# Optimization experiments

Hardware: AMD Instinct MI355X
Metric: run time of the kernel (lower is better)

## Reference

```python
import jax, jax.numpy as jnp
import numpy as np

B, C, D = 4, 2048, 1024
DCONV, DMAMBA, K, DSTATE = 512, 512, 4, 16
FFN = 2560


def setup_inputs() -> dict:
    key = jax.random.key(0)
    ks = jax.random.split(key, 16)
    n = lambda k, shape, s=1.0: jax.random.normal(k, shape, jnp.float32) * s
    inv = lambda f: 1.0 / float(np.sqrt(f))
    return {
        "x": n(ks[0], (B, C, D)),
        "velocity": n(ks[1], (B, C, D), 0.1),
        "v_hat_chunk": n(ks[2], (B, C, D)),
        "delta_W": n(ks[3], (FFN, D), 0.01),
        "pre_norm_w": jnp.ones((D,), jnp.float32),
        "ffn_norm_w": jnp.ones((D,), jnp.float32),
        "conv_in_w": n(ks[4], (D, 2 * DCONV), inv(D)),
        "conv_kernel_w": n(ks[5], (K, 1, DCONV), inv(K)),
        "ssm_in_w": n(ks[6], (D, 2 * DMAMBA), inv(D)),
        "ssm_dt_w": n(ks[7], (D, DMAMBA), inv(D)),
        "ssm_dt_b": jnp.full((DMAMBA,), -4.0, jnp.float32),
        "ssm_A_log": jnp.tile(jnp.log(jnp.arange(1.0, DSTATE + 1, dtype=jnp.float32)), (DMAMBA, 1)),
        "ssm_B_w": n(ks[8], (D, DSTATE), inv(D)),
        "ssm_C_w": n(ks[9], (D, DSTATE), inv(D)),
        "ssm_D": jnp.ones((DMAMBA,), jnp.float32),
        "out_proj_w": n(ks[10], (D, D), inv(D)),
        "log_beta": jnp.array(0.0, jnp.float32),  # sigmoid -> beta=0.5
        "ffn_gate_up_w": n(ks[11], (D, 2 * FFN), inv(D)),
        "ffn_down_w": n(ks[12], (FFN, D), inv(FFN)),
        "ffn_target_w": n(ks[13], (D, FFN), inv(D)),
        "log_gamma": jnp.array(0.0, jnp.float32),
        "log_eta": jnp.array(-4.0, jnp.float32),
    }


def _rms(x, w, eps=1e-6):
    return x * jax.lax.rsqrt(jnp.mean(x * x, axis=-1, keepdims=True) + eps) * w


def _gated_conv(xn, w_in, kernel):
    # proj -> split gate/value, depthwise causal conv on value, silu-gate
    g, v = jnp.split(xn @ w_in, 2, axis=-1)  # (B,C,DCONV) each
    v = jax.lax.conv_general_dilated(
        v, kernel, window_strides=(1,), padding=[(K - 1, 0)],
        dimension_numbers=("NWC", "WIO", "NWC"), feature_group_count=DCONV)
    return jax.nn.silu(g) * v


def _ssm(xn, w_in, w_dt, dt_b, A_log, w_B, w_C, Dp):
    # Mamba-style selective SISO scan
    u, z = jnp.split(xn @ w_in, 2, axis=-1)          # (B,C,DMAMBA)
    dt = jax.nn.softplus(xn @ w_dt + dt_b)            # (B,C,DMAMBA)
    A = -jnp.exp(A_log)                               # (DMAMBA,DSTATE)
    Bs = xn @ w_B                                     # (B,C,DSTATE)
    Cs = xn @ w_C                                     # (B,C,DSTATE)
    dA = jnp.exp(dt[..., None] * A)                   # (B,C,DMAMBA,DSTATE)
    dBu = (dt * u)[..., None] * Bs[:, :, None, :]     # (B,C,DMAMBA,DSTATE)

    def step(h, inputs):
        dA_t, dBu_t, C_t = inputs
        h = dA_t * h + dBu_t                          # (B,DMAMBA,DSTATE)
        return h, jnp.einsum("bds,bs->bd", h, C_t)

    xs = (jnp.moveaxis(dA, 1, 0), jnp.moveaxis(dBu, 1, 0), jnp.moveaxis(Cs, 1, 0))
    _, ys = jax.lax.scan(step, jnp.zeros((B, DMAMBA, DSTATE), xn.dtype), xs)
    y = jnp.moveaxis(ys, 0, 1) + Dp * u               # (B,C,DMAMBA)
    return y * jax.nn.silu(z)


def reference(x, velocity, v_hat_chunk, delta_W, pre_norm_w, ffn_norm_w,
              conv_in_w, conv_kernel_w, ssm_in_w, ssm_dt_w, ssm_dt_b, ssm_A_log,
              ssm_B_w, ssm_C_w, ssm_D, out_proj_w, log_beta, ffn_gate_up_w,
              ffn_down_w, ffn_target_w, log_gamma, log_eta):
    xn = _rms(x, pre_norm_w)
    conv_out = _gated_conv(xn, conv_in_w, conv_kernel_w)
    ssm_out = _ssm(xn, ssm_in_w, ssm_dt_w, ssm_dt_b, ssm_A_log, ssm_B_w, ssm_C_w, ssm_D)
    mixed = jnp.concatenate([conv_out, ssm_out], axis=-1) @ out_proj_w
    # momentum residual
    velocity = jax.nn.sigmoid(log_beta) * velocity + mixed
    x = x + velocity
    # Living SwiGLU
    ffn_in = _rms(x, ffn_norm_w)
    gate, up = jnp.split(ffn_in @ ffn_gate_up_w, 2, axis=-1)
    z = jax.nn.silu(gate) * up                        # (B,C,FFN)
    out = z @ ffn_down_w + z @ delta_W                # fast-weight augmented down proj
    v_hat_proj = v_hat_chunk @ ffn_target_w           # (B,C,FFN)
    update = jnp.einsum("bcf,bcd->fd", v_hat_proj, ffn_in) / x.shape[0]
    new_delta_W = jax.nn.sigmoid(log_gamma) * delta_W + jax.nn.softplus(log_eta) * update
    x = x + out
    return (x, velocity, new_delta_W)
```

## Files before the change

kernel.cpp:

```cpp
#include <hip/hip_runtime.h>
#include <stdint.h>
#include <stddef.h>

#define B_ 4
#define C_ 2048
#define D_ 1024
#define FFN_ 2560
#define ROWS_ 8192

typedef unsigned short u16;
typedef short bf16x8 __attribute__((ext_vector_type(8)));
typedef float f32x4 __attribute__((ext_vector_type(4)));

__device__ __forceinline__ float bf2f(u16 x){ union { unsigned u; float f; } v; v.u = ((unsigned)x)<<16; return v.f; }
__device__ __forceinline__ u16 f2bf(float f){ union { float f; unsigned u; } v; v.f = f; unsigned r = v.u + 0x7fffu + ((v.u>>16)&1u); return (u16)(r>>16); }
__device__ __forceinline__ float sigm_(float x){ return 1.f/(1.f+__expf(-x)); }
__device__ __forceinline__ float silu_(float x){ return x/(1.f+__expf(-x)); }
__device__ __forceinline__ float softplus_(float x){ return (x>15.f)? x : log1pf(__expf(x)); }

__device__ __forceinline__ void async16(u16* lds_base, const u16* g){
  __builtin_amdgcn_global_load_lds((const __attribute__((address_space(1))) unsigned int*)g,
                                   (__attribute__((address_space(3))) unsigned int*)lds_base,
                                   16, 0, 0);
}

#define EPI_INPROJ 0
#define EPI_MOM    1
#define EPI_SWIGLU 2
#define EPI_TRANS  3
#define EPI_ATOMX  4
#define EPI_ATOMD  5

template<int EPI>
__global__ __launch_bounds__(256)
void gemm128(const u16* __restrict__ A, const u16* __restrict__ Bt,
             int M, int N, int K, int ksplit,
             float* __restrict__ f0, float* __restrict__ f1,
             const float* __restrict__ c0, const float* __restrict__ c1, const float* __restrict__ c2,
             u16* __restrict__ h0, u16* __restrict__ h1)
{
  __shared__ u16 As[128*32];
  __shared__ u16 Bs[128*32];
  const int tid  = threadIdx.x;
  const int wave = tid>>6, lane = tid&63;
  const int bm = blockIdx.y*128, bn = blockIdx.x*128;
  const int srow = wave*32 + (lane>>2);
  const int scol = (lane&3)*8;
  const u16* aG0 = A  + (size_t)(bm + srow)*K + scol;
  const u16* aG1 = aG0 + (size_t)16*K;
  const u16* bG0 = Bt + (size_t)(bn + srow)*K + scol;
  const u16* bG1 = bG0 + (size_t)16*K;
  u16* aL0 = As + (wave*2+0)*512;
  u16* aL1 = As + (wave*2+1)*512;
  u16* bL0 = Bs + (wave*2+0)*512;
  u16* bL1 = Bs + (wave*2+1)*512;
  const int wr = wave>>1, wc = wave&1;
  const int mrow = lane&15, quad = lane>>4;

  f32x4 acc[4][4];
  #pragma unroll
  for (int i=0;i<4;i++)
    #pragma unroll
    for (int j=0;j<4;j++) acc[i][j] = (f32x4){0.f,0.f,0.f,0.f};

  const int kbeg = blockIdx.z * ksplit;
  const int kend = kbeg + ksplit;
  for (int k0=kbeg; k0<kend; k0+=32){
    __syncthreads();
    async16(aL0, aG0 + k0);
    async16(aL1, aG1 + k0);
    async16(bL0, bG0 + k0);
    async16(bL1, bG1 + k0);
    __syncthreads();
    bf16x8 af[4], bfv[4];
    #pragma unroll
    for (int i=0;i<4;i++) af[i]  = *(const bf16x8*)(As + (wr*64+i*16+mrow)*32 + quad*8);
    #pragma unroll
    for (int j=0;j<4;j++) bfv[j] = *(const bf16x8*)(Bs + (wc*64+j*16+mrow)*32 + quad*8);
    #pragma unroll
    for (int i=0;i<4;i++)
      #pragma unroll
      for (int j=0;j<4;j++)
        acc[i][j] = __builtin_amdgcn_mfma_f32_16x16x32_bf16(af[i], bfv[j], acc[i][j], 0,0,0);
  }

  #pragma unroll
  for (int i=0;i<4;i++){
    const int row0 = bm + wr*64 + i*16 + quad*4;
    #pragma unroll
    for (int j=0;j<4;j++){
      const int col = bn + wc*64 + j*16 + mrow;
      f32x4 v = acc[i][j];
      if constexpr (EPI == EPI_INPROJ){
        if (col < 1024){
          #pragma unroll
          for (int t=0;t<4;t++) h0[(size_t)(row0+t)*1024 + col] = f2bf(v[t]);
        } else if (col < 2048){
          #pragma unroll
          for (int t=0;t<4;t++) h1[(size_t)(row0+t)*1024 + (col-1024)] = f2bf(v[t]);
        } else if (col < 2560){
          const float b = c0[col-2048];
          #pragma unroll
          for (int t=0;t<4;t++) f0[(size_t)(row0+t)*512 + (col-2048)] = softplus_(v[t]+b);
        } else {
          const int cl = col - 2560;
          if (cl < 32){
            #pragma unroll
            for (int t=0;t<4;t++) f1[(size_t)(row0+t)*32 + cl] = v[t];
          }
        }
      } else if constexpr (EPI == EPI_MOM){
        const float beta = sigm_(c2[0]);
        #pragma unroll
        for (int t=0;t<4;t++){
          size_t idx = (size_t)(row0+t)*N + col;
          float vel = beta*c0[idx] + v[t];
          f0[idx] = vel;
          f1[idx] = c1[idx] + vel;
        }
      } else if constexpr (EPI == EPI_SWIGLU){
        float pv[4];
        #pragma unroll
        for (int t=0;t<4;t++) pv[t] = __shfl_xor(v[t], 1, 64);
        if (!(mrow & 1)){
          const int o = col >> 1;
          #pragma unroll
          for (int t=0;t<4;t++) h0[(size_t)(row0+t)*2560 + o] = f2bf(silu_(v[t])*pv[t]);
        }
      } else if constexpr (EPI == EPI_TRANS){
        ushort4 p; p.x=f2bf(v[0]); p.y=f2bf(v[1]); p.z=f2bf(v[2]); p.w=f2bf(v[3]);
        *(ushort4*)(h0 + (size_t)col*M + row0) = p;
      } else if constexpr (EPI == EPI_ATOMX){
        #pragma unroll
        for (int t=0;t<4;t++) atomicAdd(&f0[(size_t)(row0+t)*N + col], v[t]);
      } else if constexpr (EPI == EPI_ATOMD){
        const float e = softplus_(c2[0])*0.25f;
        #pragma unroll
        for (int t=0;t<4;t++) atomicAdd(&f0[(size_t)(row0+t)*N + col], e*v[t]);
      }
    }
  }
}

__global__ void transpose_cvt(const float* __restrict__ W, u16* __restrict__ Wt, int K, int N)
{
  __shared__ float tile[32][33];
  const int tx = threadIdx.x, ty = threadIdx.y;
  const int c0 = blockIdx.x*32, r0 = blockIdx.y*32;
  #pragma unroll
  for (int i=0;i<4;i++) tile[ty+8*i][tx] = W[(size_t)(r0+ty+8*i)*N + c0+tx];
  __syncthreads();
  #pragma unroll
  for (int i=0;i<4;i++) Wt[(size_t)(c0+ty+8*i)*K + r0+tx] = f2bf(tile[tx][ty+8*i]);
}

__global__ void transpose_cvt_gu(const float* __restrict__ W, u16* __restrict__ Wt)
{
  __shared__ float tile[32][33];
  const int tx = threadIdx.x, ty = threadIdx.y;
  const int c0 = blockIdx.x*32, r0 = blockIdx.y*32;
  #pragma unroll
  for (int i=0;i<4;i++) tile[ty+8*i][tx] = W[(size_t)(r0+ty+8*i)*5120 + c0+tx];
  __syncthreads();
  #pragma unroll
  for (int i=0;i<4;i++){
    const int c = c0+ty+8*i;
    const int n = (c < 2560) ? (c*2) : ((c-2560)*2+1);
    Wt[(size_t)n*1024 + r0+tx] = f2bf(tile[tx][ty+8*i]);
  }
}

__global__ void bcw_cvt(const float* __restrict__ Bw, const float* __restrict__ Cw, u16* __restrict__ out)
{
  int i = blockIdx.x*256 + threadIdx.x;
  int r = i >> 10, k = i & 1023;
  float v = 0.f;
  if (r < 16) v = Bw[k*16 + r];
  else if (r < 32) v = Cw[k*16 + (r-16)];
  out[(size_t)r*1024 + k] = f2bf(v);
}

__global__ void weff_transpose(const float* __restrict__ Wa, const float* __restrict__ Wb, u16* __restrict__ Wt)
{
  __shared__ float tile[32][33];
  const int tx = threadIdx.x, ty = threadIdx.y;
  const int c0 = blockIdx.x*32, r0 = blockIdx.y*32;
  #pragma unroll
  for (int i=0;i<4;i++){
    size_t idx = (size_t)(r0+ty+8*i)*1024 + c0+tx;
    tile[ty+8*i][tx] = Wa[idx] + Wb[idx];
  }
  __syncthreads();
  #pragma unroll
  for (int i=0;i<4;i++) Wt[(size_t)(c0+ty+8*i)*2560 + r0+tx] = f2bf(tile[tx][ty+8*i]);
}

__global__ void transpose_bf16(const u16* __restrict__ in, u16* __restrict__ out, int R, int Cc)
{
  __shared__ u16 tile[32][33];
  const int tx = threadIdx.x, ty = threadIdx.y;
  const int c0 = blockIdx.x*32, r0 = blockIdx.y*32;
  #pragma unroll
  for (int i=0;i<4;i++) tile[ty+8*i][tx] = in[(size_t)(r0+ty+8*i)*Cc + c0+tx];
  __syncthreads();
  #pragma unroll
  for (int i=0;i<4;i++) out[(size_t)(c0+ty+8*i)*R + r0+tx] = tile[tx][ty+8*i];
}

__global__ void cvt_bf16x4(const float* __restrict__ in, u16* __restrict__ out, int n4)
{
  int i = blockIdx.x*256 + threadIdx.x;
  if (i < n4){
    float4 v = ((const float4*)in)[i];
    ushort4 p; p.x=f2bf(v.x); p.y=f2bf(v.y); p.z=f2bf(v.z); p.w=f2bf(v.w);
    ((ushort4*)out)[i] = p;
  }
}

__global__ void atab_k(const float* __restrict__ A_log, float* __restrict__ A_tab)
{
  int i = blockIdx.x*256 + threadIdx.x;
  if (i < 512*16) A_tab[i] = -__expf(A_log[i]);
}

__global__ void delta_init(const float* __restrict__ dW, const float* __restrict__ lg, float* __restrict__ out)
{
  int i = blockIdx.x*256 + threadIdx.x;
  float g = sigm_(lg[0]);
  float4 v = ((const float4*)dW)[i];
  float4 r; r.x=g*v.x; r.y=g*v.y; r.z=g*v.z; r.w=g*v.w;
  ((float4*)out)[i] = r;
}

__global__ __launch_bounds__(256) void rmsnorm_k(const float* __restrict__ x, const float* __restrict__ w, u16* __restrict__ out)
{
  const int row = blockIdx.x, tid = threadIdx.x;
  float4 v = ((const float4*)(x + (size_t)row*1024))[tid];
  float s = v.x*v.x + v.y*v.y + v.z*v.z + v.w*v.w;
  #pragma unroll
  for (int o=32;o>0;o>>=1) s += __shfl_down(s, o);
  __shared__ float red[4];
  const int wave = tid>>6, lane = tid&63;
  if (lane==0) red[wave] = s;
  __syncthreads();
  float tot = red[0]+red[1]+red[2]+red[3];
  float sc = rsqrtf(tot*(1.f/1024.f) + 1e-6f);
  float4 wv = ((const float4*)w)[tid];
  ushort4 p; p.x=f2bf(v.x*sc*wv.x); p.y=f2bf(v.y*sc*wv.y); p.z=f2bf(v.z*sc*wv.z); p.w=f2bf(v.w*sc*wv.w);
  ((ushort4*)(out + (size_t)row*1024))[tid] = p;
}

__global__ __launch_bounds__(256) void conv_k(const u16* __restrict__ P1, const float* __restrict__ kw, u16* __restrict__ mixed)
{
  const int idx = blockIdx.x*256 + threadIdx.x;
  const int c = idx & 511;
  const int t = (idx>>9) & 2047;
  const int b = idx >> 20;
  const size_t rowb = (size_t)b*2048;
  float g = bf2f(P1[(rowb+t)*1024 + c]);
  float acc = 0.f;
  #pragma unroll
  for (int k=0;k<4;k++){
    int tt = t-3+k;
    if (tt>=0) acc += bf2f(P1[(rowb+tt)*1024 + 512 + c]) * kw[k*512+c];
  }
  mixed[(rowb+t)*1024 + c] = f2bf(silu_(g)*acc);
}

__global__ __launch_bounds__(256) void scan_p1(const float* __restrict__ dt, const u16* __restrict__ P2,
                                               const float* __restrict__ BCs, const float* __restrict__ A_tab,
                                               float* __restrict__ hend, float* __restrict__ aprod)
{
  const int d = blockIdx.x*256 + threadIdx.x;
  const int ch = blockIdx.y, b = blockIdx.z;
  float Ar[16], h[16], ap[16];
  #pragma unroll
  for (int s=0;s<16;s++){ Ar[s] = A_tab[d*16+s]; h[s]=0.f; ap[s]=1.f; }
  const int t0 = ch*128;
  for (int t=0;t<128;t++){
    size_t row = (size_t)b*2048 + t0 + t;
    float dtv = dt[row*512 + d];
    float u = bf2f(P2[row*1024 + d]);
    float du = dtv*u;
    const float* bs = BCs + row*32;
    #pragma unroll
    for (int s=0;s<16;s++){
      float dA = __expf(dtv*Ar[s]);
      h[s] = dA*h[s] + du*bs[s];
      ap[s] *= dA;
    }
  }
  size_t o = ((size_t)((b*512+d)*16 + ch))*16;
  #pragma unroll
  for (int s=0;s<16;s++){ hend[o+s]=h[s]; aprod[o+s]=ap[s]; }
}

__global__ __launch_bounds__(256) void scan_p2(const float* __restrict__ hend, const float* __restrict__ aprod,
                                               float* __restrict__ hin)
{
  const int g = blockIdx.x*256 + threadIdx.x;
  const int s = g & 15, bd = g >> 4;
  float h = 0.f;
  for (int ch=0; ch<16; ch++){
    size_t o = ((size_t)(bd*16+ch))*16 + s;
    hin[o] = h;
    h = aprod[o]*h + hend[o];
  }
}

__global__ __launch_bounds__(256) void scan_p3(const float* __restrict__ dt, const u16* __restrict__ P2,
                                               const float* __restrict__ BCs, const float* __restrict__ A_tab,
                                               const float* __restrict__ hin, const float* __restrict__ Dp,
                                               u16* __restrict__ mixed)
{
  const int d = blockIdx.x*256 + threadIdx.x;
  const int ch = blockIdx.y, b = blockIdx.z;
  float Ar[16], h[16];
  size_t o = ((size_t)((b*512+d)*16 + ch))*16;
  #pragma unroll
  for (int s=0;s<16;s++){ Ar[s] = A_tab[d*16+s]; h[s] = hin[o+s]; }
  const float Dd = Dp[d];
  const int t0 = ch*128;
  for (int t=0;t<128;t++){
    size_t row = (size_t)b*2048 + t0 + t;
    float dtv = dt[row*512 + d];
    float u = bf2f(P2[row*1024 + d]);
    float zv = bf2f(P2[row*1024 + 512 + d]);
    float du = dtv*u;
    const float* bs = BCs + row*32;
    const float* cs = bs + 16;
    float y = 0.f;
    #pragma unroll
    for (int s=0;s<16;s++){
      float dA = __expf(dtv*Ar[s]);
      h[s] = dA*h[s] + du*bs[s];
      y += h[s]*cs[s];
    }
    float outv = (y + Dd*u)*silu_(zv);
    mixed[row*1024 + 512 + d] = f2bf(outv);
  }
}

extern "C" void kernel_launch(void* const* d_in, const int* in_sizes, int n_in,
                              void* d_out, int out_size, void* d_ws, size_t ws_size,
                              hipStream_t stream)
{
  const float* x          = (const float*)d_in[0];
  const float* velocity   = (const float*)d_in[1];
  const float* v_hat      = (const float*)d_in[2];
  const float* delta_W    = (const float*)d_in[3];
  const float* pre_norm_w = (const float*)d_in[4];
  const float* ffn_norm_w = (const float*)d_in[5];
  const float* conv_in_w  = (const float*)d_in[6];
  const float* conv_kw    = (const float*)d_in[7];
  const float* ssm_in_w   = (const float*)d_in[8];
  const float* ssm_dt_w   = (const float*)d_in[9];
  const float* ssm_dt_b   = (const float*)d_in[10];
  const float* ssm_A_log  = (const float*)d_in[11];
  const float* ssm_B_w    = (const float*)d_in[12];
  const float* ssm_C_w    = (const float*)d_in[13];
  const float* ssm_D      = (const float*)d_in[14];
  const float* out_proj_w = (const float*)d_in[15];
  const float* log_beta   = (const float*)d_in[16];
  const float* gate_up_w  = (const float*)d_in[17];
  const float* ffn_down_w = (const float*)d_in[18];
  const float* ffn_tgt_w  = (const float*)d_in[19];
  const float* log_gamma  = (const float*)d_in[20];
  const float* log_eta    = (const float*)d_in[21];

  float* out_x     = (float*)d_out;
  float* out_vel   = out_x + (size_t)ROWS_*D_;
  float* out_delta = out_vel + (size_t)ROWS_*D_;

  char* wsp = (char*)d_ws;
  size_t off = 0;
  auto alloc = [&](size_t bytes)->char*{ char* p = wsp + off; off += (bytes + 255) & ~(size_t)255; return p; };

  u16* Wti        = (u16*)alloc((size_t)2688*1024*2);
  u16* out_proj_t = (u16*)alloc((size_t)1024*1024*2);
  u16* gate_up_t  = (u16*)alloc((size_t)5120*1024*2);
  u16* target_t   = (u16*)alloc((size_t)2560*1024*2);
  u16* weff_t     = (u16*)alloc((size_t)1024*2560*2);
  float* A_tab    = (float*)alloc((size_t)512*16*4);
  u16* xn         = (u16*)alloc((size_t)ROWS_*1024*2);
  u16* P1         = (u16*)alloc((size_t)ROWS_*1024*2);
  u16* P2         = (u16*)alloc((size_t)ROWS_*1024*2);
  float* dtbuf    = (float*)alloc((size_t)ROWS_*512*4);
  float* BCs      = (float*)alloc((size_t)ROWS_*32*4);
  float* hend     = (float*)alloc((size_t)4*512*16*16*4);
  float* aprod    = (float*)alloc((size_t)4*512*16*16*4);
  float* hin      = (float*)alloc((size_t)4*512*16*16*4);
  u16* mixed      = (u16*)alloc((size_t)ROWS_*1024*2);
  u16* ffn_in     = (u16*)alloc((size_t)ROWS_*1024*2);
  u16* zbuf       = (u16*)alloc((size_t)ROWS_*2560*2);
  u16* T1t        = (u16*)alloc((size_t)2560*ROWS_*2);
  u16* ffn_inT    = xn;
  u16* vhat_bf    = P1;

  dim3 tb(32,8);
  transpose_cvt<<<dim3(32,32),  tb, 0, stream>>>(conv_in_w,  Wti,                    1024, 1024);
  transpose_cvt<<<dim3(32,32),  tb, 0, stream>>>(ssm_in_w,   Wti + (size_t)1024*1024,1024, 1024);
  transpose_cvt<<<dim3(16,32),  tb, 0, stream>>>(ssm_dt_w,   Wti + (size_t)2048*1024,1024, 512);
  bcw_cvt<<<512, 256, 0, stream>>>(ssm_B_w, ssm_C_w, Wti + (size_t)2560*1024);
  transpose_cvt<<<dim3(32,32),  tb, 0, stream>>>(out_proj_w, out_proj_t, 1024, 1024);
  transpose_cvt_gu<<<dim3(160,32), tb, 0, stream>>>(gate_up_w, gate_up_t);
  transpose_cvt<<<dim3(80,32),  tb, 0, stream>>>(ffn_tgt_w,  target_t,  1024, 2560);
  weff_transpose<<<dim3(32,80), tb, 0, stream>>>(ffn_down_w, delta_W, weff_t);
  atab_k<<<32, 256, 0, stream>>>(ssm_A_log, A_tab);
  delta_init<<<2560, 256, 0, stream>>>(delta_W, log_gamma, out_delta);

  rmsnorm_k<<<ROWS_, 256, 0, stream>>>(x, pre_norm_w, xn);
  gemm128<EPI_INPROJ><<<dim3(21,64), 256, 0, stream>>>(xn, Wti, ROWS_,2688,1024,1024,
      dtbuf, BCs, ssm_dt_b, nullptr, nullptr, P1, P2);

  conv_k<<<16384, 256, 0, stream>>>(P1, conv_kw, mixed);
  scan_p1<<<dim3(2,16,4), 256, 0, stream>>>(dtbuf, P2, BCs, A_tab, hend, aprod);
  scan_p2<<<128, 256, 0, stream>>>(hend, aprod, hin);
  scan_p3<<<dim3(2,16,4), 256, 0, stream>>>(dtbuf, P2, BCs, A_tab, hin, ssm_D, mixed);

  gemm128<EPI_MOM><<<dim3(8,64), 256, 0, stream>>>(mixed, out_proj_t, ROWS_,1024,1024,1024,
      out_vel, out_x, velocity, x, log_beta, nullptr, nullptr);

  rmsnorm_k<<<ROWS_, 256, 0, stream>>>(out_x, ffn_norm_w, ffn_in);
  transpose_bf16<<<dim3(32,256), tb, 0, stream>>>(ffn_in, ffn_inT, ROWS_, 1024);
  cvt_bf16x4<<<8192, 256, 0, stream>>>(v_hat, vhat_bf, ROWS_*1024/4);

  gemm128<EPI_SWIGLU><<<dim3(40,64), 256, 0, stream>>>(ffn_in, gate_up_t, ROWS_,5120,1024,1024,
      nullptr,nullptr,nullptr,nullptr,nullptr, zbuf, nullptr);
  gemm128<EPI_TRANS><<<dim3(20,64), 256, 0, stream>>>(vhat_bf, target_t, ROWS_,2560,1024,1024,
      nullptr,nullptr,nullptr,nullptr,nullptr, T1t, nullptr);

  gemm128<EPI_ATOMX><<<dim3(8,64,2), 256, 0, stream>>>(zbuf, weff_t, ROWS_,1024,2560,1280,
      out_x,nullptr,nullptr,nullptr,nullptr, nullptr,nullptr);

  gemm128<EPI_ATOMD><<<dim3(8,20,8), 256, 0, stream>>>(T1t, ffn_inT, 2560,1024,ROWS_,1024,
      out_delta,nullptr,nullptr,nullptr, log_eta, nullptr,nullptr);
}
```

Measured before the change: 979.5 us.

## Shorten scan chunks, stage transposed GEMM epilogue through LDS, merge prep kernels

New measurement: 882.3 us. 9.9% less time.

```diff
diff --git a/kernel.cpp b/kernel.cpp
--- a/kernel.cpp
+++ b/kernel.cpp
@@ -39,8 +39,9 @@
              const float* __restrict__ c0, const float* __restrict__ c1, const float* __restrict__ c2,
              u16* __restrict__ h0, u16* __restrict__ h1)
 {
-  __shared__ u16 As[128*32];
-  __shared__ u16 Bs[128*32];
+  __shared__ u16 smem[8192];
+  u16* As = smem;
+  u16* Bs = smem + 4096;
   const int tid  = threadIdx.x;
   const int wave = tid>>6, lane = tid&63;
   const int bm = blockIdx.y*128, bn = blockIdx.x*128;
@@ -84,100 +85,128 @@
         acc[i][j] = __builtin_amdgcn_mfma_f32_16x16x32_bf16(af[i], bfv[j], acc[i][j], 0,0,0);
   }
 
-  #pragma unroll
-  for (int i=0;i<4;i++){
-    const int row0 = bm + wr*64 + i*16 + quad*4;
-    #pragma unroll
-    for (int j=0;j<4;j++){
-      const int col = bn + wc*64 + j*16 + mrow;
-      f32x4 v = acc[i][j];
-      if constexpr (EPI == EPI_INPROJ){
-        if (col < 1024){
+  if constexpr (EPI == EPI_TRANS){
+    __syncthreads();
+    #pragma unroll
+    for (int h=0; h<4; h++){
+      const int hw = h>>1, j0 = (h&1)*2;
+      if (wc == hw){
+        #pragma unroll
+        for (int i=0;i<4;i++){
+          const int rbase = wr*64 + i*16 + quad*4;
           #pragma unroll
-          for (int t=0;t<4;t++) h0[(size_t)(row0+t)*1024 + col] = f2bf(v[t]);
-        } else if (col < 2048){
-          #pragma unroll
-          for (int t=0;t<4;t++) h1[(size_t)(row0+t)*1024 + (col-1024)] = f2bf(v[t]);
-        } else if (col < 2560){
-          const float b = c0[col-2048];
-          #pragma unroll
-          for (int t=0;t<4;t++) f0[(size_t)(row0+t)*512 + (col-2048)] = softplus_(v[t]+b);
-        } else {
-          const int cl = col - 2560;
-          if (cl < 32){
+          for (int jj=0;jj<2;jj++){
+            const int j = j0+jj;
+            const int cl = jj*16 + mrow;
+            f32x4 v = acc[i][j];
             #pragma unroll
-            for (int t=0;t<4;t++) f1[(size_t)(row0+t)*32 + cl] = v[t];
+            for (int t=0;t<4;t++) smem[cl*132 + rbase + t] = f2bf(v[t]);
           }
         }
-      } else if constexpr (EPI == EPI_MOM){
-        const float beta = sigm_(c2[0]);
+      }
+      __syncthreads();
+      {
+        const int cl2 = tid>>3, m0 = (tid&7)*16;
+        const int col = bn + h*32 + cl2;
+        const ushort4* s4 = (const ushort4*)(smem + cl2*132 + m0);
+        ushort4* d4 = (ushort4*)(h0 + (size_t)col*M + bm + m0);
         #pragma unroll
-        for (int t=0;t<4;t++){
-          size_t idx = (size_t)(row0+t)*N + col;
-          float vel = beta*c0[idx] + v[t];
-          f0[idx] = vel;
-          f1[idx] = c1[idx] + vel;
+        for (int q=0;q<4;q++) d4[q] = s4[q];
+      }
+      __syncthreads();
+    }
+  } else {
+    #pragma unroll
+    for (int i=0;i<4;i++){
+      const int row0 = bm + wr*64 + i*16 + quad*4;
+      if constexpr (EPI == EPI_SWIGLU){
+        #pragma unroll
+        for (int jp=0;jp<4;jp+=2){
+          f32x4 g = acc[i][jp];
+          f32x4 u = acc[i][jp+1];
+          const int o = (((bn + wc*64 + jp*16)>>5)<<4) + mrow;
+          #pragma unroll
+          for (int t=0;t<4;t++) h0[(size_t)(row0+t)*2560 + o] = f2bf(silu_(g[t])*u[t]);
         }
-      } else if constexpr (EPI == EPI_SWIGLU){
-        float pv[4];
+      } else {
         #pragma unroll
-        for (int t=0;t<4;t++) pv[t] = __shfl_xor(v[t], 1, 64);
-        if (!(mrow & 1)){
-          const int o = col >> 1;
-          #pragma unroll
-          for (int t=0;t<4;t++) h0[(size_t)(row0+t)*2560 + o] = f2bf(silu_(v[t])*pv[t]);
+        for (int j=0;j<4;j++){
+          const int col = bn + wc*64 + j*16 + mrow;
+          f32x4 v = acc[i][j];
+          if constexpr (EPI == EPI_INPROJ){
+            if (col < 1024){
+              #pragma unroll
+              for (int t=0;t<4;t++) h0[(size_t)(row0+t)*1024 + col] = f2bf(v[t]);
+            } else if (col < 2048){
+              #pragma unroll
+              for (int t=0;t<4;t++) h1[(size_t)(row0+t)*1024 + (col-1024)] = f2bf(v[t]);
+            } else if (col < 2560){
+              const float b = c0[col-2048];
+              #pragma unroll
+              for (int t=0;t<4;t++) f0[(size_t)(row0+t)*512 + (col-2048)] = softplus_(v[t]+b);
+            } else {
+              const int cl = col - 2560;
+              if (cl < 32){
+                #pragma unroll
+                for (int t=0;t<4;t++) f1[(size_t)(row0+t)*32 + cl] = v[t];
+              }
+            }
+          } else if constexpr (EPI == EPI_MOM){
+            const float beta = sigm_(c2[0]);
+            #pragma unroll
+            for (int t=0;t<4;t++){
+              size_t idx = (size_t)(row0+t)*N + col;
+              float vel = beta*c0[idx] + v[t];
+              f0[idx] = vel;
+              f1[idx] = c1[idx] + vel;
+            }
+          } else if constexpr (EPI == EPI_ATOMX){
+            #pragma unroll
+            for (int t=0;t<4;t++) atomicAdd(&f0[(size_t)(row0+t)*N + col], v[t]);
+          } else if constexpr (EPI == EPI_ATOMD){
+            const float e = softplus_(c2[0])*0.25f;
+            #pragma unroll
+            for (int t=0;t<4;t++) atomicAdd(&f0[(size_t)(row0+t)*N + col], e*v[t]);
+          }
         }
-      } else if constexpr (EPI == EPI_TRANS){
-        ushort4 p; p.x=f2bf(v[0]); p.y=f2bf(v[1]); p.z=f2bf(v[2]); p.w=f2bf(v[3]);
-        *(ushort4*)(h0 + (size_t)col*M + row0) = p;
-      } else if constexpr (EPI == EPI_ATOMX){
-        #pragma unroll
-        for (int t=0;t<4;t++) atomicAdd(&f0[(size_t)(row0+t)*N + col], v[t]);
-      } else if constexpr (EPI == EPI_ATOMD){
-        const float e = softplus_(c2[0])*0.25f;
-        #pragma unroll
-        for (int t=0;t<4;t++) atomicAdd(&f0[(size_t)(row0+t)*N + col], e*v[t]);
       }
     }
   }
 }
 
-__global__ void transpose_cvt(const float* __restrict__ W, u16* __restrict__ Wt, int K, int N)
-{
+__global__ void prep_transposes(const float* __restrict__ conv_in_w, const float* __restrict__ ssm_in_w,
+                                const float* __restrict__ ssm_dt_w, const float* __restrict__ out_proj_w,
+                                const float* __restrict__ ffn_tgt_w, const float* __restrict__ gate_up_w,
+                                u16* __restrict__ Wti, u16* __restrict__ out_proj_t,
+                                u16* __restrict__ target_t, u16* __restrict__ gate_up_t)
+{
+  const int z = blockIdx.z;
+  const float* W; u16* Wt; int N; bool gu = false;
+  switch(z){
+    case 0: W=conv_in_w;  Wt=Wti;                       N=1024; break;
+    case 1: W=ssm_in_w;   Wt=Wti + (size_t)1024*1024;   N=1024; break;
+    case 2: W=ssm_dt_w;   Wt=Wti + (size_t)2048*1024;   N=512;  break;
+    case 3: W=out_proj_w; Wt=out_proj_t;                N=1024; break;
+    case 4: W=ffn_tgt_w;  Wt=target_t;                  N=2560; break;
+    default: W=gate_up_w; Wt=gate_up_t;                 N=5120; gu=true; break;
+  }
+  const int c0 = blockIdx.x*32, r0 = blockIdx.y*32;
+  if (c0 >= N) return;
   __shared__ float tile[32][33];
   const int tx = threadIdx.x, ty = threadIdx.y;
-  const int c0 = blockIdx.x*32, r0 = blockIdx.y*32;
   #pragma unroll
   for (int i=0;i<4;i++) tile[ty+8*i][tx] = W[(size_t)(r0+ty+8*i)*N + c0+tx];
   __syncthreads();
   #pragma unroll
-  for (int i=0;i<4;i++) Wt[(size_t)(c0+ty+8*i)*K + r0+tx] = f2bf(tile[tx][ty+8*i]);
-}
-
-__global__ void transpose_cvt_gu(const float* __restrict__ W, u16* __restrict__ Wt)
-{
-  __shared__ float tile[32][33];
-  const int tx = threadIdx.x, ty = threadIdx.y;
-  const int c0 = blockIdx.x*32, r0 = blockIdx.y*32;
-  #pragma unroll
-  for (int i=0;i<4;i++) tile[ty+8*i][tx] = W[(size_t)(r0+ty+8*i)*5120 + c0+tx];
-  __syncthreads();
-  #pragma unroll
   for (int i=0;i<4;i++){
     const int c = c0+ty+8*i;
-    const int n = (c < 2560) ? (c*2) : ((c-2560)*2+1);
+    int n;
+    if (gu){
+      if (c < 2560) n = ((c>>4)<<5) | (c&15);
+      else { int o = c-2560; n = ((o>>4)<<5) | 16 | (o&15); }
+    } else n = c;
     Wt[(size_t)n*1024 + r0+tx] = f2bf(tile[tx][ty+8*i]);
   }
-}
-
-__global__ void bcw_cvt(const float* __restrict__ Bw, const float* __restrict__ Cw, u16* __restrict__ out)
-{
-  int i = blockIdx.x*256 + threadIdx.x;
-  int r = i >> 10, k = i & 1023;
-  float v = 0.f;
-  if (r < 16) v = Bw[k*16 + r];
-  else if (r < 32) v = Cw[k*16 + (r-16)];
-  out[(size_t)r*1024 + k] = f2bf(v);
 }
 
 __global__ void weff_transpose(const float* __restrict__ Wa, const float* __restrict__ Wb, u16* __restrict__ Wt)
@@ -217,19 +246,30 @@
   }
 }
 
-__global__ void atab_k(const float* __restrict__ A_log, float* __restrict__ A_tab)
-{
-  int i = blockIdx.x*256 + threadIdx.x;
-  if (i < 512*16) A_tab[i] = -__expf(A_log[i]);
-}
-
-__global__ void delta_init(const float* __restrict__ dW, const float* __restrict__ lg, float* __restrict__ out)
-{
-  int i = blockIdx.x*256 + threadIdx.x;
-  float g = sigm_(lg[0]);
-  float4 v = ((const float4*)dW)[i];
-  float4 r; r.x=g*v.x; r.y=g*v.y; r.z=g*v.z; r.w=g*v.w;
-  ((float4*)out)[i] = r;
+__global__ void prep_small(const float* __restrict__ dW, const float* __restrict__ lg,
+                           const float* __restrict__ Bw, const float* __restrict__ Cw,
+                           const float* __restrict__ A_log,
+                           float* __restrict__ out_delta, u16* __restrict__ bc_dst,
+                           float* __restrict__ A_tab)
+{
+  const int blk = blockIdx.x, tid = threadIdx.x;
+  if (blk < 2560){
+    int i = blk*256 + tid;
+    float g = sigm_(lg[0]);
+    float4 v = ((const float4*)dW)[i];
+    float4 r; r.x=g*v.x; r.y=g*v.y; r.z=g*v.z; r.w=g*v.w;
+    ((float4*)out_delta)[i] = r;
+  } else if (blk < 3072){
+    int i = (blk-2560)*256 + tid;
+    int r = i >> 10, k = i & 1023;
+    float v = 0.f;
+    if (r < 16) v = Bw[k*16 + r];
+    else if (r < 32) v = Cw[k*16 + (r-16)];
+    bc_dst[(size_t)r*1024 + k] = f2bf(v);
+  } else {
+    int i = (blk-3072)*256 + tid;
+    if (i < 512*16) A_tab[i] = -__expf(A_log[i]);
+  }
 }
 
 __global__ __launch_bounds__(256) void rmsnorm_k(const float* __restrict__ x, const float* __restrict__ w, u16* __restrict__ out)
@@ -267,6 +307,8 @@
   mixed[(rowb+t)*1024 + c] = f2bf(silu_(g)*acc);
 }
 
+#define NCH_ 64
+#define CHL_ 32
 __global__ __launch_bounds__(256) void scan_p1(const float* __restrict__ dt, const u16* __restrict__ P2,
                                                const float* __restrict__ BCs, const float* __restrict__ A_tab,
                                                float* __restrict__ hend, float* __restrict__ aprod)
@@ -276,8 +318,8 @@
   float Ar[16], h[16], ap[16];
   #pragma unroll
   for (int s=0;s<16;s++){ Ar[s] = A_tab[d*16+s]; h[s]=0.f; ap[s]=1.f; }
-  const int t0 = ch*128;
-  for (int t=0;t<128;t++){
+  const int t0 = ch*CHL_;
+  for (int t=0;t<CHL_;t++){
     size_t row = (size_t)b*2048 + t0 + t;
     float dtv = dt[row*512 + d];
     float u = bf2f(P2[row*1024 + d]);
@@ -290,21 +332,21 @@
       ap[s] *= dA;
     }
   }
-  size_t o = ((size_t)((b*512+d)*16 + ch))*16;
+  size_t o = ((size_t)((b*512+d)*NCH_ + ch))*16;
   #pragma unroll
   for (int s=0;s<16;s++){ hend[o+s]=h[s]; aprod[o+s]=ap[s]; }
 }
 
-__global__ __launch_bounds__(256) void scan_p2(const float* __restrict__ hend, const float* __restrict__ aprod,
-                                               float* __restrict__ hin)
+__global__ __launch_bounds__(256) void scan_p2(float* __restrict__ hend, const float* __restrict__ aprod)
 {
   const int g = blockIdx.x*256 + threadIdx.x;
   const int s = g & 15, bd = g >> 4;
   float h = 0.f;
-  for (int ch=0; ch<16; ch++){
-    size_t o = ((size_t)(bd*16+ch))*16 + s;
-    hin[o] = h;
-    h = aprod[o]*h + hend[o];
+  for (int ch=0; ch<NCH_; ch++){
+    size_t o = ((size_t)(bd*NCH_+ch))*16 + s;
+    float he = hend[o], ap = aprod[o];
+    hend[o] = h;
+    h = ap*h + he;
   }
 }
 
@@ -316,12 +358,12 @@
   const int d = blockIdx.x*256 + threadIdx.x;
   const int ch = blockIdx.y, b = blockIdx.z;
   float Ar[16], h[16];
-  size_t o = ((size_t)((b*512+d)*16 + ch))*16;
+  size_t o = ((size_t)((b*512+d)*NCH_ + ch))*16;
   #pragma unroll
   for (int s=0;s<16;s++){ Ar[s] = A_tab[d*16+s]; h[s] = hin[o+s]; }
   const float Dd = Dp[d];
-  const int t0 = ch*128;
-  for (int t=0;t<128;t++){
+  const int t0 = ch*CHL_;
+  for (int t=0;t<CHL_;t++){
     size_t row = (size_t)b*2048 + t0 + t;
     float dtv = dt[row*512 + d];
     float u = bf2f(P2[row*1024 + d]);
@@ -387,9 +429,8 @@
   u16* P2         = (u16*)alloc((size_t)ROWS_*1024*2);
   float* dtbuf    = (float*)alloc((size_t)ROWS_*512*4);
   float* BCs      = (float*)alloc((size_t)ROWS_*32*4);
-  float* hend     = (float*)alloc((size_t)4*512*16*16*4);
-  float* aprod    = (float*)alloc((size_t)4*512*16*16*4);
-  float* hin      = (float*)alloc((size_t)4*512*16*16*4);
+  float* hend     = (float*)alloc((size_t)4*512*NCH_*16*4);
+  float* aprod    = (float*)alloc((size_t)4*512*NCH_*16*4);
   u16* mixed      = (u16*)alloc((size_t)ROWS_*1024*2);
   u16* ffn_in     = (u16*)alloc((size_t)ROWS_*1024*2);
   u16* zbuf       = (u16*)alloc((size_t)ROWS_*2560*2);
@@ -398,25 +439,20 @@
   u16* vhat_bf    = P1;
 
   dim3 tb(32,8);
-  transpose_cvt<<<dim3(32,32),  tb, 0, stream>>>(conv_in_w,  Wti,                    1024, 1024);
-  transpose_cvt<<<dim3(32,32),  tb, 0, stream>>>(ssm_in_w,   Wti + (size_t)1024*1024,1024, 1024);
-  transpose_cvt<<<dim3(16,32),  tb, 0, stream>>>(ssm_dt_w,   Wti + (size_t)2048*1024,1024, 512);
-  bcw_cvt<<<512, 256, 0, stream>>>(ssm_B_w, ssm_C_w, Wti + (size_t)2560*1024);
-  transpose_cvt<<<dim3(32,32),  tb, 0, stream>>>(out_proj_w, out_proj_t, 1024, 1024);
-  transpose_cvt_gu<<<dim3(160,32), tb, 0, stream>>>(gate_up_w, gate_up_t);
-  transpose_cvt<<<dim3(80,32),  tb, 0, stream>>>(ffn_tgt_w,  target_t,  1024, 2560);
+  prep_transposes<<<dim3(160,32,6), tb, 0, stream>>>(conv_in_w, ssm_in_w, ssm_dt_w, out_proj_w,
+      ffn_tgt_w, gate_up_w, Wti, out_proj_t, target_t, gate_up_t);
   weff_transpose<<<dim3(32,80), tb, 0, stream>>>(ffn_down_w, delta_W, weff_t);
-  atab_k<<<32, 256, 0, stream>>>(ssm_A_log, A_tab);
-  delta_init<<<2560, 256, 0, stream>>>(delta_W, log_gamma, out_delta);
+  prep_small<<<3104, 256, 0, stream>>>(delta_W, log_gamma, ssm_B_w, ssm_C_w, ssm_A_log,
+      out_delta, Wti + (size_t)2560*1024, A_tab);
 
   rmsnorm_k<<<ROWS_, 256, 0, stream>>>(x, pre_norm_w, xn);
   gemm128<EPI_INPROJ><<<dim3(21,64), 256, 0, stream>>>(xn, Wti, ROWS_,2688,1024,1024,
       dtbuf, BCs, ssm_dt_b, nullptr, nullptr, P1, P2);
 
   conv_k<<<16384, 256, 0, stream>>>(P1, conv_kw, mixed);
-  scan_p1<<<dim3(2,16,4), 256, 0, stream>>>(dtbuf, P2, BCs, A_tab, hend, aprod);
-  scan_p2<<<128, 256, 0, stream>>>(hend, aprod, hin);
-  scan_p3<<<dim3(2,16,4), 256, 0, stream>>>(dtbuf, P2, BCs, A_tab, hin, ssm_D, mixed);
+  scan_p1<<<dim3(2,NCH_,4), 256, 0, stream>>>(dtbuf, P2, BCs, A_tab, hend, aprod);
+  scan_p2<<<128, 256, 0, stream>>>(hend, aprod);
+  scan_p3<<<dim3(2,NCH_,4), 256, 0, stream>>>(dtbuf, P2, BCs, A_tab, hend, ssm_D, mixed);
 
   gemm128<EPI_MOM><<<dim3(8,64), 256, 0, stream>>>(mixed, out_proj_t, ROWS_,1024,1024,1024,
       out_vel, out_x, velocity, x, log_beta, nullptr, nullptr);
```
